# Performance work log

Measured on AMD Instinct MI355X. Metric: run time of the kernel, lower is better.

Reference implementation:

```python
import jax, jax.numpy as jnp
import numpy as np

DIM = 384
HEADS = 6
NEG = -1e9  # masked-score fill; equivalent to gathering only kept K/V rows


def setup_inputs() -> dict:
    key = jax.random.key(0)
    ks = jax.random.split(key, 9)
    B, N, C = 1, 4098, DIM
    x = jax.random.normal(ks[0], (B, N, C), dtype=jnp.float32)
    pos = jax.random.normal(ks[1], (B, N + 1, C), dtype=jnp.float32)
    # float mask in [0,1); >=0.5 means 'foreground / keep as key', <0.5 pooled into back token
    mask = jax.random.uniform(ks[2], (B, 1, N - 2), dtype=jnp.float32)
    mask_block = jnp.ones((N + 1,), dtype=jnp.float32)  # positions 0, N-1, N always kept
    Wq = jax.random.normal(ks[3], (C, C), dtype=jnp.float32) * 0.02
    Wk = jax.random.normal(ks[4], (C, C), dtype=jnp.float32) * 0.02
    Wv = jax.random.normal(ks[5], (C, C), dtype=jnp.float32) * 0.02
    Wp = jax.random.normal(ks[6], (C, C), dtype=jnp.float32) * 0.02
    bp = jnp.zeros((C,), dtype=jnp.float32)
    return {"x": x, "pos": pos, "mask": mask, "mask_block": mask_block,
            "Wq": Wq, "Wk": Wk, "Wv": Wv, "Wp": Wp, "bp": bp}


def reference(x, pos, mask, mask_block, Wq, Wk, Wv, Wp, bp):
    B, N, C = x.shape
    H = HEADS
    D = C // H
    scale = D ** -0.5
    eps = 1e-10

    # back token: average of background (mask < 0.5) interior tokens
    reverse = jnp.where(mask < 0.5, 1.0, 0.0)                      # (B,1,N-2)
    pooled = jnp.einsum('bon,bnc->boc', reverse, x[:, 1:N - 1])    # (B,1,C)
    back_tokens = pooled / (reverse.sum(axis=2, keepdims=True) + eps)

    kv_x = jnp.concatenate([x, back_tokens], axis=1)               # (B,N+1,C)
    q_x = x + pos[:, :N]
    k_x = kv_x + pos

    q = (q_x @ Wq.T).reshape(B, N, H, D).transpose(0, 2, 1, 3)       # (B,H,N,D)
    k = (k_x @ Wk.T).reshape(B, N + 1, H, D).transpose(0, 2, 1, 3)   # (B,H,N+1,D)
    v = (kv_x @ Wv.T).reshape(B, N + 1, H, D).transpose(0, 2, 1, 3)  # (B,H,N+1,D)

    # key-selection mask: original gathers rows with mask_block >= 0.5;
    # masked softmax over all N+1 keys is mathematically identical.
    mb = mask_block.at[1:N - 1].set(mask[0, 0])
    keep = mb >= 0.5                                               # (N+1,)

    scores = jnp.einsum('bhqd,bhkd->bhqk', q, k) * scale
    scores = jnp.where(keep[None, None, None, :], scores, NEG)
    attn = jax.nn.softmax(scores, axis=-1)
    out = jnp.einsum('bhqk,bhkd->bhqd', attn, v)
    out = out.transpose(0, 2, 1, 3).reshape(B, N, C)
    return out @ Wp.T + bp
```

## Files before the change

kernel.cpp:

```cpp
#include <hip/hip_runtime.h>
#include <math.h>

#define N_TOK 4098
#define NK_TOK 4099
#define C_DIM 384
#define NKPAD 4160

typedef short  bh8 __attribute__((ext_vector_type(8)));
typedef float  f32x4 __attribute__((ext_vector_type(4)));
typedef unsigned short ushort;
typedef ushort u4 __attribute__((ext_vector_type(4)));
typedef ushort u8 __attribute__((ext_vector_type(8)));

static __device__ __forceinline__ ushort f2bf(float f) {
  unsigned int u = __float_as_uint(f);
  u = (u + 0x7FFF + ((u >> 16) & 1)) >> 16;
  return (ushort)u;
}
static __device__ __forceinline__ float bf2f(ushort s) {
  return __uint_as_float(((unsigned int)s) << 16);
}

__global__ __launch_bounds__(384) void pool_kernel(
    const float* __restrict__ x, const float* __restrict__ mask,
    float* __restrict__ pooled_part, float* __restrict__ cnt_part) {
  const int b = blockIdx.x, t = threadIdx.x;
  const int r0 = b * 32;
  float acc = 0.f;
  int lc = 0;
  for (int r = r0; r < r0 + 32; ++r)
    if (mask[r] < 0.5f) { acc += x[(size_t)(r + 1) * C_DIM + t]; ++lc; }
  pooled_part[b * C_DIM + t] = acc;
  if (t == 0) cnt_part[b] = (float)lc;
}

__global__ __launch_bounds__(256) void prep_kernel(
    const float* __restrict__ x, const float* __restrict__ pos,
    const float* __restrict__ pooled_part, const float* __restrict__ cnt_part,
    const float* __restrict__ Wq, const float* __restrict__ Wk,
    const float* __restrict__ Wv, const float* __restrict__ Wp,
    const float* __restrict__ mask, const float* __restrict__ mask_block,
    ushort* __restrict__ Aq, ushort* __restrict__ Ak, ushort* __restrict__ Av,
    ushort* __restrict__ Wb, int* __restrict__ nk, int* __restrict__ inv) {
  const int b = blockIdx.x, t = threadIdx.x;
  if (b < 260) {
    __shared__ float sback[C_DIM];
    if (b == 256) {
      float cs = 0.f;
      for (int i = (t & 63); i < 128; i += 64) cs += cnt_part[i];
#pragma unroll
      for (int d = 1; d < 64; d <<= 1) cs += __shfl_xor(cs, d);
      const float ic = 1.f / (cs + 1e-10f);
      for (int c = t; c < C_DIM; c += 256) {
        float s = 0.f;
        for (int p = 0; p < 128; ++p) s += pooled_part[p * C_DIM + c];
        sback[c] = s * ic;
      }
      __syncthreads();
    }
    const int r0 = b * 16;
#pragma unroll
    for (int i = 0; i < 6; ++i) {
      const int idx = i * 1024 + t * 4;
      const int row = r0 + idx / C_DIM, col = idx % C_DIM;
      if (row >= NK_TOK) continue;
      const float4 pv = *(const float4*)&pos[(size_t)row * C_DIM + col];
      float4 xv;
      if (row == NK_TOK - 1)
        xv = make_float4(sback[col], sback[col + 1], sback[col + 2], sback[col + 3]);
      else
        xv = *(const float4*)&x[(size_t)row * C_DIM + col];
      if (row < N_TOK) {
        u4 q4 = {f2bf((xv.x + pv.x) * 0.125f), f2bf((xv.y + pv.y) * 0.125f),
                 f2bf((xv.z + pv.z) * 0.125f), f2bf((xv.w + pv.w) * 0.125f)};
        *(u4*)&Aq[(size_t)row * C_DIM + col] = q4;
      }
      u4 k4 = {f2bf(xv.x + pv.x), f2bf(xv.y + pv.y),
               f2bf(xv.z + pv.z), f2bf(xv.w + pv.w)};
      *(u4*)&Ak[(size_t)row * C_DIM + col] = k4;
      u4 v4 = {f2bf(xv.x), f2bf(xv.y), f2bf(xv.z), f2bf(xv.w)};
      *(u4*)&Av[(size_t)row * C_DIM + col] = v4;
    }
  } else if (b < 292) {
    const int wi = b - 260;
    const float* src = (wi < 8) ? Wq : (wi < 16) ? Wk : (wi < 24) ? Wv : Wp;
    const int base = (wi >> 3) * 147456 + (wi & 7) * 18432;
#pragma unroll 2
    for (int i = 0; i < 18; ++i) {
      const int g = base + i * 1024 + t * 4;
      const float4 v = *(const float4*)&src[(wi & 7) * 18432 + i * 1024 + t * 4];
      u4 o = {f2bf(v.x), f2bf(v.y), f2bf(v.z), f2bf(v.w)};
      *(u4*)&Wb[g] = o;
    }
  } else {
    __shared__ int scnt[256];
    const int j0 = t * 17;
    unsigned int bits = 0;
    int c = 0;
#pragma unroll 1
    for (int u = 0; u < 17; ++u) {
      const int j = j0 + u;
      bool keep = false;
      if (j < NK_TOK)
        keep = (j >= 1 && j <= N_TOK - 2) ? (mask[j - 1] >= 0.5f)
                                          : (mask_block[j] >= 0.5f);
      if (keep) { bits |= 1u << u; ++c; }
    }
    scnt[t] = c;
    __syncthreads();
    for (int d = 1; d < 256; d <<= 1) {
      const int v = scnt[t];
      const int add = (t >= d) ? scnt[t - d] : 0;
      __syncthreads();
      scnt[t] = v + add;
      __syncthreads();
    }
    int base = scnt[t] - c;
    if (t == 255) *nk = scnt[255];
#pragma unroll 1
    for (int u = 0; u < 17; ++u) {
      const int j = j0 + u;
      if (j < NK_TOK) inv[j] = ((bits >> u) & 1) ? base++ : -1;
    }
  }
}

static __device__ __forceinline__ void gemm_core(
    const ushort* __restrict__ A, const ushort* __restrict__ B,
    ushort (* __restrict__ As)[72], ushort (* __restrict__ Bs)[72],
    int t, int w, int quad, int l15, f32x4 acc[4]) {
  const int g = t & 7;
  u8 ra[2], rb[2];
#pragma unroll
  for (int it = 0; it < 2; ++it) {
    const int r = it * 32 + (t >> 3);
    ra[it] = *(const u8*)&A[r * C_DIM + g * 8];
    rb[it] = *(const u8*)&B[r * C_DIM + g * 8];
  }
#pragma unroll 1
  for (int kt = 0; kt < 6; ++kt) {
    __syncthreads();
#pragma unroll
    for (int it = 0; it < 2; ++it) {
      const int r = it * 32 + (t >> 3);
      *(u8*)&As[r][g * 8] = ra[it];
      *(u8*)&Bs[r][g * 8] = rb[it];
    }
    __syncthreads();
    if (kt < 5) {
      const int k0 = (kt + 1) * 64;
#pragma unroll
      for (int it = 0; it < 2; ++it) {
        const int r = it * 32 + (t >> 3);
        ra[it] = *(const u8*)&A[r * C_DIM + k0 + g * 8];
        rb[it] = *(const u8*)&B[r * C_DIM + k0 + g * 8];
      }
    }
    const bh8 b0 = *(const bh8*)&Bs[w * 16 + l15][quad * 8];
    const bh8 b1 = *(const bh8*)&Bs[w * 16 + l15][32 + quad * 8];
#pragma unroll
    for (int mb = 0; mb < 4; ++mb) {
      const bh8 a0 = *(const bh8*)&As[mb * 16 + l15][quad * 8];
      const bh8 a1 = *(const bh8*)&As[mb * 16 + l15][32 + quad * 8];
      acc[mb] = __builtin_amdgcn_mfma_f32_16x16x32_bf16(a0, b0, acc[mb], 0, 0, 0);
      acc[mb] = __builtin_amdgcn_mfma_f32_16x16x32_bf16(a1, b1, acc[mb], 0, 0, 0);
    }
  }
}

__global__ __launch_bounds__(256) void gemm3_kernel(
    const ushort* __restrict__ Aq, const ushort* __restrict__ Ak,
    const ushort* __restrict__ Av, const ushort* __restrict__ Wb,
    const int* __restrict__ inv, ushort* __restrict__ Qh,
    ushort* __restrict__ Kc, ushort* __restrict__ Vc) {
  __shared__ ushort As[64][72], Bs[64][72];
  const int t = threadIdx.x, w = t >> 6, lane = t & 63;
  const int quad = lane >> 4, l15 = lane & 15;
  const int m0 = blockIdx.x * 64;
  const int which = blockIdx.y / 6, h = blockIdx.y % 6;
  const ushort* A = (which == 0 ? Aq : which == 1 ? Ak : Av) + (size_t)m0 * C_DIM;
  const ushort* B = Wb + (size_t)which * 147456 + (size_t)h * 64 * C_DIM;
  f32x4 acc[4];
#pragma unroll
  for (int i = 0; i < 4; ++i) acc[i] = (f32x4){0.f, 0.f, 0.f, 0.f};
  gemm_core(A, B, As, Bs, t, w, quad, l15, acc);
  const int n = w * 16 + l15;
  if (which == 0) {
#pragma unroll
    for (int mb = 0; mb < 4; ++mb)
#pragma unroll
      for (int r = 0; r < 4; ++r) {
        const int m = m0 + mb * 16 + quad * 4 + r;
        if (m < N_TOK) Qh[((size_t)h * N_TOK + m) * 64 + n] = f2bf(acc[mb][r]);
      }
  } else {
    ushort* dst = (which == 1) ? Kc : Vc;
#pragma unroll
    for (int mb = 0; mb < 4; ++mb)
#pragma unroll
      for (int r = 0; r < 4; ++r) {
        const int m = m0 + mb * 16 + quad * 4 + r;
        if (m < NK_TOK) {
          const int slot = inv[m];
          if (slot >= 0) dst[((size_t)h * NKPAD + slot) * 64 + n] = f2bf(acc[mb][r]);
        }
      }
  }
}

__global__ __launch_bounds__(256) void gemm_out_kernel(
    const ushort* __restrict__ Am, const ushort* __restrict__ Wpb,
    const float* __restrict__ bp, float* __restrict__ out) {
  __shared__ ushort As[64][72], Bs[64][72];
  const int t = threadIdx.x, w = t >> 6, lane = t & 63;
  const int quad = lane >> 4, l15 = lane & 15;
  const int m0 = blockIdx.x * 64;
  const int h = blockIdx.y;
  f32x4 acc[4];
#pragma unroll
  for (int i = 0; i < 4; ++i) acc[i] = (f32x4){0.f, 0.f, 0.f, 0.f};
  gemm_core(Am + (size_t)m0 * C_DIM, Wpb + (size_t)h * 64 * C_DIM,
            As, Bs, t, w, quad, l15, acc);
  const int n = w * 16 + l15;
  const float bb = bp[h * 64 + n];
#pragma unroll
  for (int mb = 0; mb < 4; ++mb)
#pragma unroll
    for (int r = 0; r < 4; ++r) {
      const int m = m0 + mb * 16 + quad * 4 + r;
      if (m < N_TOK) out[(size_t)m * C_DIM + h * 64 + n] = acc[mb][r] + bb;
    }
}

__global__ __launch_bounds__(256) void vtrans_kernel(const ushort* __restrict__ Vc,
                                                     ushort* __restrict__ Vt) {
  __shared__ ushort T[64][72];
  const int c = blockIdx.x, h = blockIdx.y, t = threadIdx.x;
#pragma unroll
  for (int i = 0; i < 2; ++i) {
    const int s = t + i * 256, r = s >> 3, g = s & 7;
    *(u8*)&T[r][g * 8] =
        *(const u8*)&Vc[((size_t)h * NKPAD + c * 64 + r) * 64 + g * 8];
  }
  __syncthreads();
#pragma unroll
  for (int i = 0; i < 2; ++i) {
    const int s = t + i * 256, d = s >> 3, g = s & 7;
    u8 o;
#pragma unroll
    for (int j = 0; j < 8; ++j) o[j] = T[g * 8 + j][d];
    *(u8*)&Vt[((size_t)h * 64 + d) * NKPAD + c * 64 + g * 8] = o;
  }
}

__global__ __launch_bounds__(256) void attn_kernel(
    const ushort* __restrict__ Qh, const ushort* __restrict__ Kc,
    const ushort* __restrict__ Vt, const int* __restrict__ nkp,
    ushort* __restrict__ Opart, float* __restrict__ Lpart) {
  __shared__ ushort Ks[64][72];
  __shared__ ushort Vs[64][72];
  __shared__ ushort Ps[4][16][72];
  const int t = threadIdx.x, w = t >> 6, lane = t & 63;
  const int quad = lane >> 4, l15 = lane & 15;
  const int h = blockIdx.y, slice = blockIdx.z;
  const int q0 = blockIdx.x * 64;
  const int nk = *nkp, nchunk = (nk + 63) >> 6;
  const int g = t & 7;

  bh8 qf0, qf1;
  {
    int qr = q0 + w * 16 + l15;
    if (qr > N_TOK - 1) qr = N_TOK - 1;
    const ushort* qp = Qh + ((size_t)h * N_TOK + qr) * 64 + quad * 8;
    qf0 = *(const bh8*)qp;
    qf1 = *(const bh8*)(qp + 32);
  }
  f32x4 oacc[4];
#pragma unroll
  for (int i = 0; i < 4; ++i) oacc[i] = (f32x4){0.f, 0.f, 0.f, 0.f};
  float l_r = 0.f;

  const ushort* kb = Kc + (size_t)h * NKPAD * 64;
  const ushort* vb = Vt + (size_t)h * 64 * NKPAD;

  u8 rk[2], rv[2];
  if (slice < nchunk) {
#pragma unroll
    for (int it = 0; it < 2; ++it) {
      const int r = it * 32 + (t >> 3);
      rk[it] = *(const u8*)&kb[(size_t)(slice * 64 + r) * 64 + g * 8];
      rv[it] = *(const u8*)&vb[(size_t)r * NKPAD + slice * 64 + g * 8];
    }
  }
#pragma unroll 1
  for (int kc = slice; kc < nchunk; kc += 3) {
    __syncthreads();
#pragma unroll
    for (int it = 0; it < 2; ++it) {
      const int r = it * 32 + (t >> 3);
      *(u8*)&Ks[r][g * 8] = rk[it];
      *(u8*)&Vs[r][g * 8] = rv[it];
    }
    __syncthreads();
    if (kc + 3 < nchunk) {
#pragma unroll
      for (int it = 0; it < 2; ++it) {
        const int r = it * 32 + (t >> 3);
        rk[it] = *(const u8*)&kb[(size_t)((kc + 3) * 64 + r) * 64 + g * 8];
        rv[it] = *(const u8*)&vb[(size_t)r * NKPAD + (kc + 3) * 64 + g * 8];
      }
    }
    float csum = 0.f;
#pragma unroll
    for (int f = 0; f < 4; ++f) {
      f32x4 s4 = {0.f, 0.f, 0.f, 0.f};
      const bh8 a0 = *(const bh8*)&Ks[f * 16 + l15][quad * 8];
      const bh8 a1 = *(const bh8*)&Ks[f * 16 + l15][32 + quad * 8];
      s4 = __builtin_amdgcn_mfma_f32_16x16x32_bf16(a0, qf0, s4, 0, 0, 0);
      s4 = __builtin_amdgcn_mfma_f32_16x16x32_bf16(a1, qf1, s4, 0, 0, 0);
      const int keyb = kc * 64 + f * 16 + quad * 4;
      u4 pv;
#pragma unroll
      for (int r = 0; r < 4; ++r) {
        const float p = (keyb + r < nk) ? __expf(s4[r]) : 0.f;
        csum += p;
        pv[r] = f2bf(p);
      }
      *(u4*)&Ps[w][l15][f * 16 + quad * 4] = pv;
    }
    csum += __shfl_xor(csum, 16);
    csum += __shfl_xor(csum, 32);
    l_r += csum;

    const bh8 pa0 = *(const bh8*)&Ps[w][l15][quad * 8];
    const bh8 pa1 = *(const bh8*)&Ps[w][l15][32 + quad * 8];
#pragma unroll
    for (int db = 0; db < 4; ++db) {
      const bh8 b0 = *(const bh8*)&Vs[db * 16 + l15][quad * 8];
      const bh8 b1 = *(const bh8*)&Vs[db * 16 + l15][32 + quad * 8];
      oacc[db] = __builtin_amdgcn_mfma_f32_16x16x32_bf16(pa0, b0, oacc[db], 0, 0, 0);
      oacc[db] = __builtin_amdgcn_mfma_f32_16x16x32_bf16(pa1, b1, oacc[db], 0, 0, 0);
    }
  }

  const int sh = slice * 6 + h;
  const int qg = q0 + w * 16;
#pragma unroll
  for (int db = 0; db < 4; ++db)
#pragma unroll
    for (int r = 0; r < 4; ++r) {
      const int q = qg + quad * 4 + r;
      if (q < N_TOK)
        Opart[((size_t)sh * NKPAD + q) * 64 + db * 16 + l15] = f2bf(oacc[db][r]);
    }
  if (quad == 0) {
    const int q = qg + l15;
    if (q < N_TOK) Lpart[sh * NKPAD + q] = l_r;
  }
}

__global__ __launch_bounds__(256) void merge_kernel(const ushort* __restrict__ Opart,
                                                    const float* __restrict__ Lpart,
                                                    ushort* __restrict__ Am) {
  const int idx = blockIdx.x * 256 + threadIdx.x;
  if (idx >= N_TOK * 48) return;
  const int q = idx / 48, c = (idx % 48) * 8;
  const int h = c >> 6, d = c & 63;
  float l = 0.f;
#pragma unroll
  for (int s = 0; s < 3; ++s) l += Lpart[(s * 6 + h) * NKPAD + q];
  const float inv = 1.f / l;
  float o[8] = {0.f, 0.f, 0.f, 0.f, 0.f, 0.f, 0.f, 0.f};
#pragma unroll
  for (int s = 0; s < 3; ++s) {
    const u8 v = *(const u8*)&Opart[((size_t)(s * 6 + h) * NKPAD + q) * 64 + d];
#pragma unroll
    for (int j = 0; j < 8; ++j) o[j] += bf2f(v[j]);
  }
  u8 r;
#pragma unroll
  for (int j = 0; j < 8; ++j) r[j] = f2bf(o[j] * inv);
  *(u8*)&Am[(size_t)q * C_DIM + c] = r;
}

extern "C" void kernel_launch(void* const* d_in, const int* in_sizes, int n_in,
                              void* d_out, int out_size, void* d_ws, size_t ws_size,
                              hipStream_t stream) {
  const float* x          = (const float*)d_in[0];
  const float* pos        = (const float*)d_in[1];
  const float* mask       = (const float*)d_in[2];
  const float* mask_block = (const float*)d_in[3];
  const float* Wq         = (const float*)d_in[4];
  const float* Wk         = (const float*)d_in[5];
  const float* Wv         = (const float*)d_in[6];
  const float* Wp         = (const float*)d_in[7];
  const float* bp         = (const float*)d_in[8];
  float* out = (float*)d_out;
  char* wsb = (char*)d_ws;

  float*  pooled_part = (float*)wsb;
  float*  cnt_part    = (float*)(wsb + 196608);
  int*    nk          = (int*)(wsb + 197120);
  int*    inv         = (int*)(wsb + 197632);
  ushort* Aq          = (ushort*)(wsb + 215296);
  ushort* Ak          = (ushort*)(wsb + 3410176);
  ushort* Av          = (ushort*)(wsb + 6605056);
  ushort* Wb          = (ushort*)(wsb + 9799936);
  ushort* Qh          = (ushort*)(wsb + 10979584);
  ushort* Kc          = (ushort*)(wsb + 14126848);
  ushort* Vc          = (ushort*)(wsb + 17321728);
  ushort* Vt          = (ushort*)(wsb + 20516608);
  float*  Lp          = (float*)(wsb + 23711488);
  ushort* Am          = (ushort*)(wsb + 24011008);
  ushort* Op          = Aq;

  pool_kernel<<<dim3(128), dim3(384), 0, stream>>>(x, mask, pooled_part, cnt_part);
  prep_kernel<<<dim3(293), dim3(256), 0, stream>>>(x, pos, pooled_part, cnt_part,
                                                   Wq, Wk, Wv, Wp, mask, mask_block,
                                                   Aq, Ak, Av, Wb, nk, inv);
  gemm3_kernel<<<dim3(65, 18), 256, 0, stream>>>(Aq, Ak, Av, Wb, inv, Qh, Kc, Vc);
  vtrans_kernel<<<dim3(65, 6), 256, 0, stream>>>(Vc, Vt);
  attn_kernel<<<dim3(65, 6, 3), 256, 0, stream>>>(Qh, Kc, Vt, nk, Op, Lp);
  merge_kernel<<<dim3(769), 256, 0, stream>>>(Op, Lp, Am);
  gemm_out_kernel<<<dim3(65, 6), 256, 0, stream>>>(Am, Wb + 3 * 147456, bp, out);
}
```

Measured before the change: 158.6 us.

## Write V transposed from GEMM, widen attention query tile, use six key slices

The V projection now writes straight into the transposed Vt layout, which removes the separate transpose kernel and its extra round trip through memory. The attention kernel now handles 128 queries per block (32 per wave), so each K/V tile loaded into shared memory serves twice as many queries. Key-dimension splitting goes from 3 to 6 slices to keep the grid large, and the merge kernel now sums 6 partials. The costs are scattered 2-byte stores for V^T, more registers per thread in attention, and more partial-output traffic. Workspace offsets are rearranged so the partials get their own buffer.

```diff
diff --git a/kernel.cpp b/kernel.cpp
--- a/kernel.cpp
+++ b/kernel.cpp
@@ -5,6 +5,7 @@
 #define NK_TOK 4099
 #define C_DIM 384
 #define NKPAD 4160
+#define NSLICE 6
 
 typedef short  bh8 __attribute__((ext_vector_type(8)));
 typedef float  f32x4 __attribute__((ext_vector_type(4)));
@@ -172,7 +173,7 @@
     const ushort* __restrict__ Aq, const ushort* __restrict__ Ak,
     const ushort* __restrict__ Av, const ushort* __restrict__ Wb,
     const int* __restrict__ inv, ushort* __restrict__ Qh,
-    ushort* __restrict__ Kc, ushort* __restrict__ Vc) {
+    ushort* __restrict__ Kc, ushort* __restrict__ Vt) {
   __shared__ ushort As[64][72], Bs[64][72];
   const int t = threadIdx.x, w = t >> 6, lane = t & 63;
   const int quad = lane >> 4, l15 = lane & 15;
@@ -193,8 +194,7 @@
         const int m = m0 + mb * 16 + quad * 4 + r;
         if (m < N_TOK) Qh[((size_t)h * N_TOK + m) * 64 + n] = f2bf(acc[mb][r]);
       }
-  } else {
-    ushort* dst = (which == 1) ? Kc : Vc;
+  } else if (which == 1) {
 #pragma unroll
     for (int mb = 0; mb < 4; ++mb)
 #pragma unroll
@@ -202,7 +202,18 @@
         const int m = m0 + mb * 16 + quad * 4 + r;
         if (m < NK_TOK) {
           const int slot = inv[m];
-          if (slot >= 0) dst[((size_t)h * NKPAD + slot) * 64 + n] = f2bf(acc[mb][r]);
+          if (slot >= 0) Kc[((size_t)h * NKPAD + slot) * 64 + n] = f2bf(acc[mb][r]);
+        }
+      }
+  } else {
+#pragma unroll
+    for (int mb = 0; mb < 4; ++mb)
+#pragma unroll
+      for (int r = 0; r < 4; ++r) {
+        const int m = m0 + mb * 16 + quad * 4 + r;
+        if (m < NK_TOK) {
+          const int slot = inv[m];
+          if (slot >= 0) Vt[((size_t)h * 64 + n) * NKPAD + slot] = f2bf(acc[mb][r]);
         }
       }
   }
@@ -232,53 +243,35 @@
     }
 }
 
-__global__ __launch_bounds__(256) void vtrans_kernel(const ushort* __restrict__ Vc,
-                                                     ushort* __restrict__ Vt) {
-  __shared__ ushort T[64][72];
-  const int c = blockIdx.x, h = blockIdx.y, t = threadIdx.x;
-#pragma unroll
-  for (int i = 0; i < 2; ++i) {
-    const int s = t + i * 256, r = s >> 3, g = s & 7;
-    *(u8*)&T[r][g * 8] =
-        *(const u8*)&Vc[((size_t)h * NKPAD + c * 64 + r) * 64 + g * 8];
-  }
-  __syncthreads();
-#pragma unroll
-  for (int i = 0; i < 2; ++i) {
-    const int s = t + i * 256, d = s >> 3, g = s & 7;
-    u8 o;
-#pragma unroll
-    for (int j = 0; j < 8; ++j) o[j] = T[g * 8 + j][d];
-    *(u8*)&Vt[((size_t)h * 64 + d) * NKPAD + c * 64 + g * 8] = o;
-  }
-}
-
 __global__ __launch_bounds__(256) void attn_kernel(
     const ushort* __restrict__ Qh, const ushort* __restrict__ Kc,
     const ushort* __restrict__ Vt, const int* __restrict__ nkp,
     ushort* __restrict__ Opart, float* __restrict__ Lpart) {
   __shared__ ushort Ks[64][72];
   __shared__ ushort Vs[64][72];
-  __shared__ ushort Ps[4][16][72];
+  __shared__ ushort Ps[4][32][72];
   const int t = threadIdx.x, w = t >> 6, lane = t & 63;
   const int quad = lane >> 4, l15 = lane & 15;
   const int h = blockIdx.y, slice = blockIdx.z;
-  const int q0 = blockIdx.x * 64;
+  const int q0 = blockIdx.x * 128;
   const int nk = *nkp, nchunk = (nk + 63) >> 6;
   const int g = t & 7;
 
-  bh8 qf0, qf1;
-  {
-    int qr = q0 + w * 16 + l15;
+  bh8 qf[2][2];
+#pragma unroll
+  for (int qa = 0; qa < 2; ++qa) {
+    int qr = q0 + w * 32 + qa * 16 + l15;
     if (qr > N_TOK - 1) qr = N_TOK - 1;
     const ushort* qp = Qh + ((size_t)h * N_TOK + qr) * 64 + quad * 8;
-    qf0 = *(const bh8*)qp;
-    qf1 = *(const bh8*)(qp + 32);
-  }
-  f32x4 oacc[4];
-#pragma unroll
-  for (int i = 0; i < 4; ++i) oacc[i] = (f32x4){0.f, 0.f, 0.f, 0.f};
-  float l_r = 0.f;
+    qf[qa][0] = *(const bh8*)qp;
+    qf[qa][1] = *(const bh8*)(qp + 32);
+  }
+  f32x4 oacc[2][4];
+#pragma unroll
+  for (int qa = 0; qa < 2; ++qa)
+#pragma unroll
+    for (int i = 0; i < 4; ++i) oacc[qa][i] = (f32x4){0.f, 0.f, 0.f, 0.f};
+  float l_r[2] = {0.f, 0.f};
 
   const ushort* kb = Kc + (size_t)h * NKPAD * 64;
   const ushort* vb = Vt + (size_t)h * 64 * NKPAD;
@@ -293,7 +286,7 @@
     }
   }
 #pragma unroll 1
-  for (int kc = slice; kc < nchunk; kc += 3) {
+  for (int kc = slice; kc < nchunk; kc += NSLICE) {
     __syncthreads();
 #pragma unroll
     for (int it = 0; it < 2; ++it) {
@@ -302,60 +295,80 @@
       *(u8*)&Vs[r][g * 8] = rv[it];
     }
     __syncthreads();
-    if (kc + 3 < nchunk) {
+    if (kc + NSLICE < nchunk) {
 #pragma unroll
       for (int it = 0; it < 2; ++it) {
         const int r = it * 32 + (t >> 3);
-        rk[it] = *(const u8*)&kb[(size_t)((kc + 3) * 64 + r) * 64 + g * 8];
-        rv[it] = *(const u8*)&vb[(size_t)r * NKPAD + (kc + 3) * 64 + g * 8];
-      }
-    }
-    float csum = 0.f;
+        rk[it] = *(const u8*)&kb[(size_t)((kc + NSLICE) * 64 + r) * 64 + g * 8];
+        rv[it] = *(const u8*)&vb[(size_t)r * NKPAD + (kc + NSLICE) * 64 + g * 8];
+      }
+    }
+    float csum[2] = {0.f, 0.f};
 #pragma unroll
     for (int f = 0; f < 4; ++f) {
-      f32x4 s4 = {0.f, 0.f, 0.f, 0.f};
       const bh8 a0 = *(const bh8*)&Ks[f * 16 + l15][quad * 8];
       const bh8 a1 = *(const bh8*)&Ks[f * 16 + l15][32 + quad * 8];
-      s4 = __builtin_amdgcn_mfma_f32_16x16x32_bf16(a0, qf0, s4, 0, 0, 0);
-      s4 = __builtin_amdgcn_mfma_f32_16x16x32_bf16(a1, qf1, s4, 0, 0, 0);
+      f32x4 s4[2];
+#pragma unroll
+      for (int qa = 0; qa < 2; ++qa) {
+        s4[qa] = (f32x4){0.f, 0.f, 0.f, 0.f};
+        s4[qa] = __builtin_amdgcn_mfma_f32_16x16x32_bf16(a0, qf[qa][0], s4[qa], 0, 0, 0);
+        s4[qa] = __builtin_amdgcn_mfma_f32_16x16x32_bf16(a1, qf[qa][1], s4[qa], 0, 0, 0);
+      }
       const int keyb = kc * 64 + f * 16 + quad * 4;
-      u4 pv;
-#pragma unroll
-      for (int r = 0; r < 4; ++r) {
-        const float p = (keyb + r < nk) ? __expf(s4[r]) : 0.f;
-        csum += p;
-        pv[r] = f2bf(p);
-      }
-      *(u4*)&Ps[w][l15][f * 16 + quad * 4] = pv;
-    }
-    csum += __shfl_xor(csum, 16);
-    csum += __shfl_xor(csum, 32);
-    l_r += csum;
-
-    const bh8 pa0 = *(const bh8*)&Ps[w][l15][quad * 8];
-    const bh8 pa1 = *(const bh8*)&Ps[w][l15][32 + quad * 8];
+#pragma unroll
+      for (int qa = 0; qa < 2; ++qa) {
+        u4 pv;
+#pragma unroll
+        for (int r = 0; r < 4; ++r) {
+          const float p = (keyb + r < nk) ? __expf(s4[qa][r]) : 0.f;
+          csum[qa] += p;
+          pv[r] = f2bf(p);
+        }
+        *(u4*)&Ps[w][qa * 16 + l15][f * 16 + quad * 4] = pv;
+      }
+    }
+#pragma unroll
+    for (int qa = 0; qa < 2; ++qa) {
+      csum[qa] += __shfl_xor(csum[qa], 16);
+      csum[qa] += __shfl_xor(csum[qa], 32);
+      l_r[qa] += csum[qa];
+    }
+
+    bh8 pa[2][2];
+#pragma unroll
+    for (int qa = 0; qa < 2; ++qa) {
+      pa[qa][0] = *(const bh8*)&Ps[w][qa * 16 + l15][quad * 8];
+      pa[qa][1] = *(const bh8*)&Ps[w][qa * 16 + l15][32 + quad * 8];
+    }
 #pragma unroll
     for (int db = 0; db < 4; ++db) {
       const bh8 b0 = *(const bh8*)&Vs[db * 16 + l15][quad * 8];
       const bh8 b1 = *(const bh8*)&Vs[db * 16 + l15][32 + quad * 8];
-      oacc[db] = __builtin_amdgcn_mfma_f32_16x16x32_bf16(pa0, b0, oacc[db], 0, 0, 0);
-      oacc[db] = __builtin_amdgcn_mfma_f32_16x16x32_bf16(pa1, b1, oacc[db], 0, 0, 0);
+#pragma unroll
+      for (int qa = 0; qa < 2; ++qa) {
+        oacc[qa][db] = __builtin_amdgcn_mfma_f32_16x16x32_bf16(pa[qa][0], b0, oacc[qa][db], 0, 0, 0);
+        oacc[qa][db] = __builtin_amdgcn_mfma_f32_16x16x32_bf16(pa[qa][1], b1, oacc[qa][db], 0, 0, 0);
+      }
     }
   }
 
   const int sh = slice * 6 + h;
-  const int qg = q0 + w * 16;
-#pragma unroll
-  for (int db = 0; db < 4; ++db)
-#pragma unroll
-    for (int r = 0; r < 4; ++r) {
-      const int q = qg + quad * 4 + r;
-      if (q < N_TOK)
-        Opart[((size_t)sh * NKPAD + q) * 64 + db * 16 + l15] = f2bf(oacc[db][r]);
-    }
-  if (quad == 0) {
-    const int q = qg + l15;
-    if (q < N_TOK) Lpart[sh * NKPAD + q] = l_r;
+#pragma unroll
+  for (int qa = 0; qa < 2; ++qa) {
+    const int qg = q0 + w * 32 + qa * 16;
+#pragma unroll
+    for (int db = 0; db < 4; ++db)
+#pragma unroll
+      for (int r = 0; r < 4; ++r) {
+        const int q = qg + quad * 4 + r;
+        if (q < N_TOK)
+          Opart[((size_t)sh * NKPAD + q) * 64 + db * 16 + l15] = f2bf(oacc[qa][db][r]);
+      }
+    if (quad == 0) {
+      const int q = qg + l15;
+      if (q < N_TOK) Lpart[sh * NKPAD + q] = l_r[qa];
+    }
   }
 }
 
@@ -368,11 +381,11 @@
   const int h = c >> 6, d = c & 63;
   float l = 0.f;
 #pragma unroll
-  for (int s = 0; s < 3; ++s) l += Lpart[(s * 6 + h) * NKPAD + q];
+  for (int s = 0; s < NSLICE; ++s) l += Lpart[(s * 6 + h) * NKPAD + q];
   const float inv = 1.f / l;
   float o[8] = {0.f, 0.f, 0.f, 0.f, 0.f, 0.f, 0.f, 0.f};
 #pragma unroll
-  for (int s = 0; s < 3; ++s) {
+  for (int s = 0; s < NSLICE; ++s) {
     const u8 v = *(const u8*)&Opart[((size_t)(s * 6 + h) * NKPAD + q) * 64 + d];
 #pragma unroll
     for (int j = 0; j < 8; ++j) o[j] += bf2f(v[j]);
@@ -408,19 +421,17 @@
   ushort* Wb          = (ushort*)(wsb + 9799936);
   ushort* Qh          = (ushort*)(wsb + 10979584);
   ushort* Kc          = (ushort*)(wsb + 14126848);
-  ushort* Vc          = (ushort*)(wsb + 17321728);
-  ushort* Vt          = (ushort*)(wsb + 20516608);
-  float*  Lp          = (float*)(wsb + 23711488);
+  ushort* Vt          = (ushort*)(wsb + 17321728);
   ushort* Am          = (ushort*)(wsb + 24011008);
-  ushort* Op          = Aq;
+  ushort* Op          = (ushort*)(wsb + 27205888);
+  float*  Lp          = (float*)(wsb + 46375168);
 
   pool_kernel<<<dim3(128), dim3(384), 0, stream>>>(x, mask, pooled_part, cnt_part);
   prep_kernel<<<dim3(293), dim3(256), 0, stream>>>(x, pos, pooled_part, cnt_part,
                                                    Wq, Wk, Wv, Wp, mask, mask_block,
                                                    Aq, Ak, Av, Wb, nk, inv);
-  gemm3_kernel<<<dim3(65, 18), 256, 0, stream>>>(Aq, Ak, Av, Wb, inv, Qh, Kc, Vc);
-  vtrans_kernel<<<dim3(65, 6), 256, 0, stream>>>(Vc, Vt);
-  attn_kernel<<<dim3(65, 6, 3), 256, 0, stream>>>(Qh, Kc, Vt, nk, Op, Lp);
+  gemm3_kernel<<<dim3(65, 18), 256, 0, stream>>>(Aq, Ak, Av, Wb, inv, Qh, Kc, Vt);
+  attn_kernel<<<dim3(33, 6, NSLICE), 256, 0, stream>>>(Qh, Kc, Vt, nk, Op, Lp);
   merge_kernel<<<dim3(769), 256, 0, stream>>>(Op, Lp, Am);
   gemm_out_kernel<<<dim3(65, 6), 256, 0, stream>>>(Am, Wb + 3 * 147456, bp, out);
 }
```

Result: faster. 155.3 us (-2.1%).
